# Kernel tuning notes

Hardware: AMD Instinct MI355X
Metric: run time of the kernel (lower is better)

## Reference

```python
import jax, jax.numpy as jnp
import numpy as np

N = 100000      # nodes
E = 1600000     # edges (avg degree 16)
F_IN = 32       # node_features
F_OUT = 32      # filters
K = 2           # Chebyshev order


def setup_inputs() -> dict:
    key = jax.random.key(0)
    ks = jax.random.split(key, 8)
    x = jax.random.normal(ks[0], (N, F_IN), dtype=jnp.float32)
    edge_index = jax.random.randint(ks[1], (2, E), 0, N, dtype=jnp.int32).astype(jnp.int64)
    edge_weight = jax.random.uniform(ks[2], (E,), dtype=jnp.float32)
    s_in = 1.0 / np.sqrt(F_IN)
    s_out = 1.0 / np.sqrt(F_OUT)
    # gate order: i, f, c, o
    Wx = jax.random.normal(ks[3], (4, K, F_IN, F_OUT), dtype=jnp.float32) * s_in
    bx = jnp.zeros((4, F_OUT), dtype=jnp.float32)
    Wh = jax.random.normal(ks[4], (4, K, F_OUT, F_OUT), dtype=jnp.float32) * s_out
    bh = jnp.zeros((4, F_OUT), dtype=jnp.float32)
    wc = jax.random.normal(ks[5], (3, F_OUT), dtype=jnp.float32) * 0.1  # peephole i, f, o
    b_gate = jnp.zeros((4, F_OUT), dtype=jnp.float32)
    lin_w = jax.random.normal(ks[6], (F_OUT, 1), dtype=jnp.float32) * s_out
    lin_b = jnp.zeros((1,), dtype=jnp.float32)
    return dict(x=x, edge_index=edge_index, edge_weight=edge_weight, Wx=Wx, bx=bx,
                Wh=Wh, bh=bh, wc=wc, b_gate=b_gate, lin_w=lin_w, lin_b=lin_b)


def _cheb_norm(src, dst, w, num_nodes):
    # ChebConv 'sym' normalization with lambda_max = 2.0:
    # scaled Laplacian L_hat = L_sym - I has zero diagonal; off-diagonal entries are
    # -D^{-1/2} A D^{-1/2}. Self loops removed (equivalently: weight zeroed).
    w = jnp.where(src == dst, 0.0, w)
    deg = jax.ops.segment_sum(w, src, num_segments=num_nodes)
    dinv = jnp.where(deg > 0, jax.lax.rsqrt(jnp.where(deg > 0, deg, 1.0)), 0.0)
    return -dinv[src] * w * dinv[dst]


def _forward(x, src, dst, norm, Wx, bx, Wh, bh, wc, b_gate, lin_w, lin_b):
    n = x.shape[0]

    def cheb(inp, W, b):
        # K=2 Chebyshev conv: Tx_0 = inp, Tx_1 = L_hat @ inp (sparse gather/scatter)
        tx1 = jax.ops.segment_sum(norm[:, None] * inp[src], dst, num_segments=n)
        return inp @ W[0] + tx1 @ W[1] + b

    H = jnp.zeros((n, Wh.shape[-1]), dtype=x.dtype)
    C = jnp.zeros_like(H)
    I = jax.nn.sigmoid(cheb(x, Wx[0], bx[0]) + cheb(H, Wh[0], bh[0]) + wc[0] * C + b_gate[0])
    Fg = jax.nn.sigmoid(cheb(x, Wx[1], bx[1]) + cheb(H, Wh[1], bh[1]) + wc[1] * C + b_gate[1])
    T = jnp.tanh(cheb(x, Wx[2], bx[2]) + cheb(H, Wh[2], bh[2]) + b_gate[2])
    C = Fg * C + I * T
    O = jax.nn.sigmoid(cheb(x, Wx[3], bx[3]) + cheb(H, Wh[3], bh[3]) + wc[2] * C + b_gate[3])
    H = O * jnp.tanh(C)
    return jax.nn.relu(H) @ lin_w + lin_b  # [N, 1]


def reference(x, edge_index, edge_weight, Wx, bx, Wh, bh, wc, b_gate, lin_w, lin_b):
    src, dst = edge_index[0], edge_index[1]
    norm = _cheb_norm(src, dst, edge_weight, x.shape[0])
    return _forward(x, src, dst, norm, Wx, bx, Wh, bh, wc, b_gate, lin_w, lin_b)
```

## Files before the change

### kernel.cpp

```cpp
#include <hip/hip_runtime.h>


#define FDIM 32
#define MAX_N 100000
#define MAX_E 1600000
#define CBSH 8
#define CB 256
#define MAX_NB ((MAX_N + CB - 1) / CB)
#define NBLK 512
#define SCAN_TILE 2048
#define GNB 64

__device__ float g_deg[MAX_N];
__device__ int   g_part2[2 * MAX_NB * NBLK + 1];
__device__ int   g_blk[1024];
__device__ uint2 g_rec[MAX_E];
__device__ uint2 g_srec[MAX_E];
__device__ int   g_row[MAX_N + 1];
__device__ int   g_src2[MAX_E];
__device__ float g_nrm2[MAX_E];
__device__ float g_tx1[MAX_N * FDIM];

__global__ __launch_bounds__(256) void hist2_kernel(const int* __restrict__ ei,
                                                    int E, int n_nodes, int nbuck,
                                                    int per_blk) {
    __shared__ int hd[MAX_NB];
    __shared__ int hs[MAX_NB];
    for (int i = threadIdx.x; i < nbuck; i += 256) { hd[i] = 0; hs[i] = 0; }
    __syncthreads();
    int start = blockIdx.x * per_blk;
    int end = start + per_blk;
    if (end > E) end = E;
    for (int e = start + threadIdx.x; e < end; e += 256) {
        int s = ei[e];
        int d = ei[E + e];
        if ((unsigned)s >= (unsigned)n_nodes || (unsigned)d >= (unsigned)n_nodes) continue;
        atomicAdd(&hd[d >> CBSH], 1);
        atomicAdd(&hs[s >> CBSH], 1);
    }
    __syncthreads();
    for (int i = threadIdx.x; i < nbuck; i += 256) {
        g_part2[i * NBLK + blockIdx.x] = hd[i];
        g_part2[(nbuck + i) * NBLK + blockIdx.x] = hs[i];
    }
    if (blockIdx.x == 0 && threadIdx.x == 0)
        g_part2[2 * nbuck * NBLK] = 0;
}

__global__ __launch_bounds__(256) void scan1_kernel(int n) {
    __shared__ int sh[256];
    int tid = threadIdx.x;
    int base = blockIdx.x * SCAN_TILE + tid * 8;
    int v[8];
#pragma unroll
    for (int i = 0; i < 8; ++i) v[i] = (base + i < n) ? g_part2[base + i] : 0;
    int tsum = 0;
#pragma unroll
    for (int i = 0; i < 8; ++i) tsum += v[i];
    sh[tid] = tsum;
    __syncthreads();
    for (int off = 1; off < 256; off <<= 1) {
        int t = (tid >= off) ? sh[tid - off] : 0;
        __syncthreads();
        sh[tid] += t;
        __syncthreads();
    }
    if (tid == 255) g_blk[blockIdx.x] = sh[255];
    int run = sh[tid] - tsum;
#pragma unroll
    for (int i = 0; i < 8; ++i) {
        if (base + i < n) g_part2[base + i] = run;
        run += v[i];
    }
}

__global__ __launch_bounds__(256) void scan2_kernel(int nb) {
    __shared__ int sh[256];
    int tid = threadIdx.x;
    int base = tid * 4;
    int v[4];
#pragma unroll
    for (int i = 0; i < 4; ++i) v[i] = (base + i < nb) ? g_blk[base + i] : 0;
    int tsum = v[0] + v[1] + v[2] + v[3];
    sh[tid] = tsum;
    __syncthreads();
    for (int off = 1; off < 256; off <<= 1) {
        int t = (tid >= off) ? sh[tid - off] : 0;
        __syncthreads();
        sh[tid] += t;
        __syncthreads();
    }
    int run = sh[tid] - tsum;
#pragma unroll
    for (int i = 0; i < 4; ++i) {
        if (base + i < nb) g_blk[base + i] = run;
        run += v[i];
    }
}

__global__ void scan3_kernel(int n) {
    int off = g_blk[blockIdx.x];
    int base = blockIdx.x * SCAN_TILE + threadIdx.x * 8;
#pragma unroll
    for (int i = 0; i < 8; ++i) {
        int idx = base + i;
        if (idx < n) g_part2[idx] += off;
    }
}

__global__ __launch_bounds__(256) void scatter2_kernel(const int* __restrict__ ei,
                                                       const float* __restrict__ w,
                                                       int E, int n_nodes, int nbuck,
                                                       int per_blk) {
    __shared__ int curD[MAX_NB];
    __shared__ int curS[MAX_NB];
    for (int i = threadIdx.x; i < nbuck; i += 256) {
        curD[i] = g_part2[i * NBLK + blockIdx.x];
        curS[i] = g_part2[(nbuck + i) * NBLK + blockIdx.x];
    }
    __syncthreads();
    int start = blockIdx.x * per_blk;
    int end = start + per_blk;
    if (end > E) end = E;
    for (int e = start + threadIdx.x; e < end; e += 256) {
        int s = ei[e];
        int d = ei[E + e];
        if ((unsigned)s >= (unsigned)n_nodes || (unsigned)d >= (unsigned)n_nodes) continue;
        float w0 = (s == d) ? 0.f : w[e];
        int posD = atomicAdd(&curD[d >> CBSH], 1);
        g_rec[posD] = make_uint2(((unsigned)s << CBSH) | (unsigned)(d & (CB - 1)),
                                 __float_as_uint(w0));
        int posS = atomicAdd(&curS[s >> CBSH], 1) - E;
        g_srec[posS] = make_uint2((unsigned)(s & (CB - 1)), __float_as_uint(w0));
    }
}

__global__ __launch_bounds__(256) void deg_sum_kernel(int E, int n_nodes, int nbuck) {
    __shared__ float ldeg[CB];
    int b = blockIdx.x;
    int rs = g_part2[(nbuck + b) * NBLK] - E;
    int re = g_part2[(nbuck + b + 1) * NBLK] - E;
    ldeg[threadIdx.x] = 0.f;
    __syncthreads();
    for (int i = rs + threadIdx.x; i < re; i += 256) {
        uint2 r = g_srec[i];
        atomicAdd(&ldeg[r.x], __uint_as_float(r.y));
    }
    __syncthreads();
    int node = (b << CBSH) + threadIdx.x;
    if (node < n_nodes) {
        float dg = ldeg[threadIdx.x];
        g_deg[node] = (dg > 0.f) ? rsqrtf(dg) : 0.f;
    }
}

__global__ __launch_bounds__(256) void fine_sort_kernel(int E, int n_nodes, int nbuck) {
    __shared__ int cnt[CB];
    __shared__ int cur[CB];
    __shared__ float dv[CB];
    __shared__ int wsum[4];
    int b = blockIdx.x;
    int rs = g_part2[b * NBLK];
    int re = g_part2[(b + 1) * NBLK];
    {
        int tid = threadIdx.x;
        cnt[tid] = 0;
        int node = (b << CBSH) + tid;
        dv[tid] = (node < n_nodes) ? g_deg[node] : 0.f;
    }
    __syncthreads();
    for (int i = rs + threadIdx.x; i < re; i += 256)
        atomicAdd(&cnt[g_rec[i].x & (CB - 1)], 1);
    __syncthreads();
    {
        int tid = threadIdx.x;
        int lane = tid & 63;
        int wave = tid >> 6;
        int v = cnt[tid];
        int inc = v;
#pragma unroll
        for (int off = 1; off < 64; off <<= 1) {
            int t = __shfl_up(inc, off, 64);
            if (lane >= off) inc += t;
        }
        if (lane == 63) wsum[wave] = inc;
        __syncthreads();
        int wo = 0;
#pragma unroll
        for (int ww = 0; ww < 4; ++ww) wo += (ww < wave) ? wsum[ww] : 0;
        int start = rs + wo + (inc - v);
        cur[tid] = start;
        int node = (b << CBSH) + tid;
        if (node < n_nodes) g_row[node] = start;
    }
    if (b == nbuck - 1 && threadIdx.x == 0) g_row[n_nodes] = re;
    __syncthreads();
    for (int i = rs + threadIdx.x; i < re; i += 256) {
        uint2 r = g_rec[i];
        int s = (int)(r.x >> CBSH);
        int loc = r.x & (CB - 1);
        float nrm = -g_deg[s] * __uint_as_float(r.y) * dv[loc];
        int pos = atomicAdd(&cur[loc], 1);
        g_src2[pos] = s;
        g_nrm2[pos] = nrm;
    }
}

__global__ __launch_bounds__(256) void gather_kernel(const float* __restrict__ x,
                                                     int n_nodes) {
    int t = blockIdx.x * blockDim.x + threadIdx.x;
    int node = t >> 5;
    int f = t & 31;
    if (node >= n_nodes) return;
    int i = g_row[node];
    int end = g_row[node + 1];
    float acc = 0.f;
    for (; i + 4 <= end; i += 4) {
        int   s0 = g_src2[i],     s1 = g_src2[i + 1], s2 = g_src2[i + 2], s3 = g_src2[i + 3];
        float n0 = g_nrm2[i],     n1 = g_nrm2[i + 1], n2 = g_nrm2[i + 2], n3 = g_nrm2[i + 3];
        acc += n0 * x[s0 * FDIM + f] + n1 * x[s1 * FDIM + f]
             + n2 * x[s2 * FDIM + f] + n3 * x[s3 * FDIM + f];
    }
    for (; i < end; ++i) acc += g_nrm2[i] * x[g_src2[i] * FDIM + f];
    g_tx1[node * FDIM + f] = acc;
}

__global__ __launch_bounds__(256) void gates64_kernel(
    const float* __restrict__ x,
    const float* __restrict__ Wx, const float* __restrict__ bx,
    const float* __restrict__ bh, const float* __restrict__ wc,
    const float* __restrict__ bg, const float* __restrict__ lin_w,
    const float* __restrict__ lin_b, float* __restrict__ out, int n_nodes) {
    __shared__ float Ws[3 * 2048];
    __shared__ float xs[GNB * FDIM];
    __shared__ float ts[GNB * FDIM];

    for (int idx = threadIdx.x; idx < 2048; idx += 256) {
        Ws[idx]          = Wx[0 * 2048 + idx];
        Ws[2048 + idx]   = Wx[2 * 2048 + idx];
        Ws[4096 + idx]   = Wx[3 * 2048 + idx];
    }
    int node0 = blockIdx.x * GNB;
    for (int t = threadIdx.x; t < GNB * FDIM; t += 256) {
        int n = node0 + (t >> 5);
        int f = t & 31;
        bool ok = (n < n_nodes);
        xs[t] = ok ? x[n * FDIM + f] : 0.f;
        ts[t] = ok ? g_tx1[n * FDIM + f] : 0.f;
    }
    __syncthreads();

    int j   = threadIdx.x & 31;
    int grp = threadIdx.x >> 5;

    float ai0=0.f,ai1=0.f,ai2=0.f,ai3=0.f,ai4=0.f,ai5=0.f,ai6=0.f,ai7=0.f;
    float ac0=0.f,ac1=0.f,ac2=0.f,ac3=0.f,ac4=0.f,ac5=0.f,ac6=0.f,ac7=0.f;
    float ao0=0.f,ao1=0.f,ao2=0.f,ao3=0.f,ao4=0.f,ao5=0.f,ao6=0.f,ao7=0.f;
    const float* xr = &xs[(grp * 8) * FDIM];
    const float* tr = &ts[(grp * 8) * FDIM];
    for (int k = 0; k < 32; ++k) {
        int o0 = k * 32 + j;
        float wi0 = Ws[o0],        wi1 = Ws[1024 + o0];
        float wc0 = Ws[2048 + o0], wc1 = Ws[3072 + o0];
        float wo0 = Ws[4096 + o0], wo1 = Ws[5120 + o0];
#define GSTEP(m, AI, AC, AO)                                   \
        {   float xv = xr[m * FDIM + k], tv = tr[m * FDIM + k];\
            AI += xv * wi0 + tv * wi1;                         \
            AC += xv * wc0 + tv * wc1;                         \
            AO += xv * wo0 + tv * wo1; }
        GSTEP(0, ai0, ac0, ao0) GSTEP(1, ai1, ac1, ao1)
        GSTEP(2, ai2, ac2, ao2) GSTEP(3, ai3, ac3, ao3)
        GSTEP(4, ai4, ac4, ao4) GSTEP(5, ai5, ac5, ao5)
        GSTEP(6, ai6, ac6, ao6) GSTEP(7, ai7, ac7, ao7)
#undef GSTEP
    }

    float bi = bx[0 * 32 + j] + bh[0 * 32 + j] + bg[0 * 32 + j];
    float bc = bx[2 * 32 + j] + bh[2 * 32 + j] + bg[2 * 32 + j];
    float bo = bx[3 * 32 + j] + bh[3 * 32 + j] + bg[3 * 32 + j];
    float wcp = wc[2 * 32 + j];
    float lwj = lin_w[j];
    float lb0 = lin_b[0];

#define GOUT(m, AI, AC, AO)                                            \
    {   int n = node0 + grp * 8 + m;                                   \
        float I = 1.f / (1.f + __expf(-(AI + bi)));                    \
        float T = tanhf(AC + bc);                                      \
        float C = I * T;                                               \
        float O = 1.f / (1.f + __expf(-(AO + bo + wcp * C)));          \
        float H = O * tanhf(C);                                        \
        float r = fmaxf(H, 0.f) * lwj;                                 \
        _Pragma("unroll")                                              \
        for (int mm = 16; mm > 0; mm >>= 1) r += __shfl_xor(r, mm, 32);\
        if (j == 0 && n < n_nodes) out[n] = r + lb0; }
    GOUT(0, ai0, ac0, ao0) GOUT(1, ai1, ac1, ao1)
    GOUT(2, ai2, ac2, ao2) GOUT(3, ai3, ac3, ao3)
    GOUT(4, ai4, ac4, ao4) GOUT(5, ai5, ac5, ao5)
    GOUT(6, ai6, ac6, ao6) GOUT(7, ai7, ac7, ao7)
#undef GOUT
}

extern "C" void kernel_launch(void* const* d_in, const int* in_sizes, int n_in,
                              void* d_out, int out_size, void* d_ws, size_t ws_size,
                              hipStream_t stream) {
    const float* x     = (const float*)d_in[0];
    const int*   ei    = (const int*)d_in[1];
    const float* w     = (const float*)d_in[2];
    const float* Wx    = (const float*)d_in[3];
    const float* bx    = (const float*)d_in[4];
    const float* bh    = (const float*)d_in[6];
    const float* wc    = (const float*)d_in[7];
    const float* bg    = (const float*)d_in[8];
    const float* lin_w = (const float*)d_in[9];
    const float* lin_b = (const float*)d_in[10];
    float*       out   = (float*)d_out;

    int n_nodes = in_sizes[0] / FDIM;
    if (n_nodes > MAX_N) n_nodes = MAX_N;
    int E = in_sizes[2];
    if (E > MAX_E) E = MAX_E;

    int nbuck   = (n_nodes + CB - 1) >> CBSH;
    int per_blk = (E + NBLK - 1) / NBLK;
    int n_scan  = 2 * nbuck * NBLK + 1;
    int nb_scan = (n_scan + SCAN_TILE - 1) / SCAN_TILE;

    hist2_kernel<<<NBLK, 256, 0, stream>>>(ei, E, n_nodes, nbuck, per_blk);
    scan1_kernel<<<nb_scan, 256, 0, stream>>>(n_scan);
    scan2_kernel<<<1, 256, 0, stream>>>(nb_scan);
    scan3_kernel<<<nb_scan, 256, 0, stream>>>(n_scan);
    scatter2_kernel<<<NBLK, 256, 0, stream>>>(ei, w, E, n_nodes, nbuck, per_blk);
    deg_sum_kernel<<<nbuck, 256, 0, stream>>>(E, n_nodes, nbuck);
    fine_sort_kernel<<<nbuck, 256, 0, stream>>>(E, n_nodes, nbuck);
    {
        long long tot = (long long)n_nodes * 32;
        gather_kernel<<<(int)((tot + 255) / 256), 256, 0, stream>>>(x, n_nodes);
    }
    gates64_kernel<<<(n_nodes + GNB - 1) / GNB, 256, 0, stream>>>(
        x, Wx, bx, bh, wc, bg, lin_w, lin_b, out, n_nodes);
}
```

Before: 276.8 us.

## Stage bucketed edge records in LDS before writing contiguous runs to global

Replaces the direct atomic-slot scatter of edge records with a block-local counting sort. Each block scans its per-bucket counts, writes records into an LDS staging buffer ordered by bucket, then streams them out so neighbouring threads write neighbouring global addresses. The goal is to turn scattered 8-byte global stores into short coalesced runs. In exchange, the edge list is read twice (once per destination/source phase), the block gains a 512-wide scan, and the kernel needs about 45KB of LDS, which lowers occupancy.

New measurement: 258.4 us. 1.07x faster.

```diff
diff --git a/kernel.cpp b/kernel.cpp
--- a/kernel.cpp
+++ b/kernel.cpp
@@ -10,6 +10,7 @@
 #define NBLK 512
 #define SCAN_TILE 2048
 #define GNB 64
+#define PERBLK 3136
 
 __device__ float g_deg[MAX_N];
 __device__ int   g_part2[2 * MAX_NB * NBLK + 1];
@@ -108,30 +109,65 @@
     }
 }
 
-__global__ __launch_bounds__(256) void scatter2_kernel(const int* __restrict__ ei,
-                                                       const float* __restrict__ w,
-                                                       int E, int n_nodes, int nbuck,
-                                                       int per_blk) {
-    __shared__ int curD[MAX_NB];
-    __shared__ int curS[MAX_NB];
-    for (int i = threadIdx.x; i < nbuck; i += 256) {
-        curD[i] = g_part2[i * NBLK + blockIdx.x];
-        curS[i] = g_part2[(nbuck + i) * NBLK + blockIdx.x];
-    }
-    __syncthreads();
-    int start = blockIdx.x * per_blk;
+__global__ __launch_bounds__(256) void scatter_burst_kernel(const int* __restrict__ ei,
+                                                            const float* __restrict__ w,
+                                                            int E, int n_nodes, int nbuck,
+                                                            int per_blk) {
+    __shared__ int   cnt[512];
+    __shared__ int   sc[512];
+    __shared__ int   gb[MAX_NB];
+    __shared__ int   cur[MAX_NB];
+    __shared__ uint2 staged[PERBLK];
+    __shared__ int   gpos[PERBLK];
+    int tid = threadIdx.x;
+    int blk = blockIdx.x;
+    int start = blk * per_blk;
     int end = start + per_blk;
     if (end > E) end = E;
-    for (int e = start + threadIdx.x; e < end; e += 256) {
-        int s = ei[e];
-        int d = ei[E + e];
-        if ((unsigned)s >= (unsigned)n_nodes || (unsigned)d >= (unsigned)n_nodes) continue;
-        float w0 = (s == d) ? 0.f : w[e];
-        int posD = atomicAdd(&curD[d >> CBSH], 1);
-        g_rec[posD] = make_uint2(((unsigned)s << CBSH) | (unsigned)(d & (CB - 1)),
-                                 __float_as_uint(w0));
-        int posS = atomicAdd(&curS[s >> CBSH], 1) - E;
-        g_srec[posS] = make_uint2((unsigned)(s & (CB - 1)), __float_as_uint(w0));
+
+    for (int phase = 0; phase < 2; ++phase) {
+        cnt[tid] = 0; cnt[tid + 256] = 0;
+        __syncthreads();
+        for (int i = tid; i < nbuck; i += 256) {
+            int flat = (phase * nbuck + i) * NBLK + blk;
+            int g0 = g_part2[flat];
+            int g1 = g_part2[flat + 1];
+            gb[i] = g0 - phase * E;
+            cnt[i] = g1 - g0;
+        }
+        __syncthreads();
+        sc[tid] = cnt[tid]; sc[tid + 256] = cnt[tid + 256];
+        __syncthreads();
+        for (int off = 1; off < 512; off <<= 1) {
+            int v0 = (tid >= off) ? sc[tid - off] : 0;
+            int v1 = sc[tid + 256 - off];
+            __syncthreads();
+            sc[tid] += v0; sc[tid + 256] += v1;
+            __syncthreads();
+        }
+        for (int i = tid; i < nbuck; i += 256) cur[i] = sc[i] - cnt[i];
+        __syncthreads();
+        for (int e = start + tid; e < end; e += 256) {
+            int s = ei[e], d = ei[E + e];
+            if ((unsigned)s >= (unsigned)n_nodes || (unsigned)d >= (unsigned)n_nodes)
+                continue;
+            int key = phase ? s : d;
+            int bin = key >> CBSH;
+            float w0 = (s == d) ? 0.f : w[e];
+            unsigned pay = phase ? (unsigned)(s & (CB - 1))
+                                 : (((unsigned)s << CBSH) | (unsigned)(d & (CB - 1)));
+            int p = atomicAdd(&cur[bin], 1);
+            staged[p] = make_uint2(pay, __float_as_uint(w0));
+            gpos[p] = gb[bin] + (p - (sc[bin] - cnt[bin]));
+        }
+        __syncthreads();
+        int tot = sc[511];
+        if (phase == 0) {
+            for (int t = tid; t < tot; t += 256) g_rec[gpos[t]] = staged[t];
+        } else {
+            for (int t = tid; t < tot; t += 256) g_srec[gpos[t]] = staged[t];
+        }
+        __syncthreads();
     }
 }
 
@@ -329,7 +365,7 @@
     scan1_kernel<<<nb_scan, 256, 0, stream>>>(n_scan);
     scan2_kernel<<<1, 256, 0, stream>>>(nb_scan);
     scan3_kernel<<<nb_scan, 256, 0, stream>>>(n_scan);
-    scatter2_kernel<<<NBLK, 256, 0, stream>>>(ei, w, E, n_nodes, nbuck, per_blk);
+    scatter_burst_kernel<<<NBLK, 256, 0, stream>>>(ei, w, E, n_nodes, nbuck, per_blk);
     deg_sum_kernel<<<nbuck, 256, 0, stream>>>(E, n_nodes, nbuck);
     fine_sort_kernel<<<nbuck, 256, 0, stream>>>(E, n_nodes, nbuck);
     {
```
